# Performance work log

Hardware: AMD Instinct MI355X
Metric: run time of the kernel (lower is better)

The kernel has to match this reference:

```python
import jax, jax.numpy as jnp
import numpy as np

NBINS = (128, 64, 32)
MIN_BIN_WIDTH = 1e-3
MIN_BIN_HEIGHT = 1e-3


def quadratic_spline(inputs, unnorm_widths, unnorm_heights):
    """Piecewise-quadratic CDF spline (nflows-style). inputs: (N,) in [0,1],
    unnorm_widths: (N, nb), unnorm_heights: (N, nb+1). Returns (outputs, logabsdet)."""
    num_bins = unnorm_widths.shape[-1]
    widths = jax.nn.softmax(unnorm_widths, axis=-1)
    widths = MIN_BIN_WIDTH + (1.0 - MIN_BIN_WIDTH * num_bins) * widths
    hexp = jnp.exp(unnorm_heights)
    # normalize piecewise-linear pdf to integrate to 1
    area = jnp.sum(0.5 * (hexp[:, :-1] + hexp[:, 1:]) * widths, axis=-1, keepdims=True)
    heights = hexp / area
    heights = MIN_BIN_HEIGHT + (1.0 - MIN_BIN_HEIGHT) * heights
    bin_cdf = jnp.cumsum(0.5 * (heights[:, :-1] + heights[:, 1:]) * widths, axis=-1)
    bin_left_cdf = jnp.pad(bin_cdf.at[:, -1].set(1.0), ((0, 0), (1, 0)))
    bin_loc = jnp.cumsum(widths, axis=-1)
    bin_locations = jnp.pad(bin_loc.at[:, -1].set(1.0), ((0, 0), (1, 0)))
    bin_idx = jnp.clip(jnp.sum((inputs[:, None] >= bin_locations).astype(jnp.int32), axis=-1) - 1,
                       0, num_bins - 1)[:, None]
    take = lambda t, i: jnp.take_along_axis(t, i, axis=-1)[:, 0]
    loc = take(bin_locations, bin_idx)
    w = take(widths, bin_idx)
    cdf = take(bin_left_cdf, bin_idx)
    hl = take(heights, bin_idx)
    hr = take(heights, bin_idx + 1)
    alpha = (inputs - loc) / w
    outputs = jnp.clip(0.5 * (hr - hl) * w * alpha * alpha + hl * w * alpha + cdf, 0.0, 1.0)
    logabsdet = jnp.log(alpha * (hr - hl) + hl)
    return outputs, logabsdet


def _forward(coordinates, clustering, delta_height_weight, delta_baseline_weight,
             unnormalized_heights, unnormalized_widths, baseline_bias,
             genes_oi, local_gene_ix, local_cellxgene_ix, localcellxgene_ix):
    n_total_genes = delta_baseline_weight.shape[0]
    # decoder
    dhw = delta_height_weight[genes_oi]                            # (G, L, K)
    mixture_delta = jnp.einsum('cl,glk->cgk', clustering, dhw)     # (C, G, K)
    baseline_delta = clustering @ delta_baseline_weight.T          # (C, n_total)
    baseline = jax.nn.softmax(jnp.log(baseline_bias)[None, :] + baseline_delta, axis=-1)
    baseline_cuts = baseline.reshape(-1)[localcellxgene_ix]        # (N,)
    delta = mixture_delta.reshape(-1, mixture_delta.shape[-1])[local_cellxgene_ix]  # (N, K)
    gene_global = genes_oi[local_gene_ix]                          # (N,)
    # quadratic spline stack log_prob (base = Uniform[0,1])
    x = coordinates
    logabsdet = jnp.zeros_like(coordinates)
    ho = 0
    wo = 0
    for n in NBINS:
        uh = unnormalized_heights[:, ho:ho + n][gene_global] + delta[:, ho:ho + n]
        uw = unnormalized_widths[:, wo:wo + n - 1][gene_global]
        x, lad = quadratic_spline(x, uw, uh)
        logabsdet = logabsdet + lad
        ho += n
        wo += n - 1
    likelihood_position = logabsdet
    likelihood_region = jnp.log(baseline_cuts) + jnp.log(jnp.asarray(n_total_genes, jnp.float32))
    elbo = -(likelihood_position + likelihood_region).sum()
    # KL regularization (scales = exp(log 1.0) = 1)
    half_log_2pi = float(0.5 * np.log(2.0 * np.pi))
    mixture_kl = -0.5 * dhw * dhw - half_log_2pi
    baseline_kl = -0.5 * jnp.square(delta_baseline_weight[genes_oi]) - half_log_2pi
    return elbo - mixture_kl.sum() - baseline_kl.sum()


def setup_inputs() -> dict:
    key = jax.random.key(0)
    ks = jax.random.split(key, 10)
    N, C, G, NT, L = 500_000, 1000, 500, 10_000, 16
    K = sum(NBINS)                # 224 heights / delta components
    W = sum(n - 1 for n in NBINS)  # 221 widths
    coordinates = jax.random.uniform(ks[0], (N,), jnp.float32, 1e-4, 1.0 - 1e-4)
    cluster_id = jax.random.randint(ks[1], (C,), 0, L)
    clustering = jax.nn.one_hot(cluster_id, L, dtype=jnp.float32)
    genes_oi = jnp.sort(jax.random.permutation(ks[2], NT)[:G]).astype(jnp.int32)
    cell_ix = jax.random.randint(ks[3], (N,), 0, C)
    local_gene_ix = jax.random.randint(ks[4], (N,), 0, G).astype(jnp.int32)
    local_cellxgene_ix = (cell_ix * G + local_gene_ix).astype(jnp.int32)
    localcellxgene_ix = (cell_ix * NT + genes_oi[local_gene_ix]).astype(jnp.int32)
    delta_height_weight = jax.random.normal(ks[5], (NT, L, K), jnp.float32) * 0.05
    delta_baseline_weight = jax.random.uniform(ks[6], (NT, L), jnp.float32, -0.25, 0.25)
    unnormalized_heights = jax.random.normal(ks[7], (NT, K), jnp.float32) * 0.1
    unnormalized_widths = jax.random.normal(ks[8], (NT, W), jnp.float32) * 0.1
    baseline_bias = jax.random.uniform(ks[9], (NT,), jnp.float32, 1e-5, 1.0)
    return {
        'coordinates': coordinates, 'clustering': clustering,
        'delta_height_weight': delta_height_weight,
        'delta_baseline_weight': delta_baseline_weight,
        'unnormalized_heights': unnormalized_heights,
        'unnormalized_widths': unnormalized_widths,
        'baseline_bias': baseline_bias,
        'genes_oi': genes_oi, 'local_gene_ix': local_gene_ix,
        'local_cellxgene_ix': local_cellxgene_ix,
        'localcellxgene_ix': localcellxgene_ix,
    }


def reference(coordinates, clustering, delta_height_weight, delta_baseline_weight,
              unnormalized_heights, unnormalized_widths, baseline_bias,
              genes_oi, local_gene_ix, local_cellxgene_ix, localcellxgene_ix):
    return _forward(coordinates, clustering, delta_height_weight, delta_baseline_weight,
                    unnormalized_heights, unnormalized_widths, baseline_bias,
                    genes_oi, local_gene_ix, local_cellxgene_ix, localcellxgene_ix)
```

## Files before the change

### kernel.cpp

```cpp
#include <hip/hip_runtime.h>
#include <math.h>


#define CAP 192
static constexpr float  F_MBW = 1e-3f;
static constexpr float  F_MBH = 1e-3f;
static constexpr double D_HL2PI = 0.918938533204672741780329736406;


__global__ void __launch_bounds__(256)
kA(const float* __restrict__ clustering, int* __restrict__ cid,
   double* __restrict__ dpart, int* __restrict__ cnt, int C, int L, int P) {
  int bid = blockIdx.x, tid = threadIdx.x;
  if (bid < 4) {
    int c = bid * 256 + tid;
    if (c < C) {
      const float* row = clustering + (size_t)c * L;
      int best = 0; float bv = row[0];
      for (int l = 1; l < L; ++l) { float v = row[l]; if (v > bv) { bv = v; best = l; } }
      cid[c] = best;
    }
  } else {
    if (bid == 4 && tid < 128) dpart[tid] = 0.0;
    int i = (bid - 4) * 256 + tid;
    if (i < P) cnt[i] = 0;
  }
}

__global__ void __launch_bounds__(256)
kB(const float* __restrict__ coords, const int* __restrict__ lgi,
   const int* __restrict__ lcg, const int* __restrict__ cid,
   const float* __restrict__ bb, const float* __restrict__ dbw,
   int* __restrict__ cnt, float* __restrict__ xs, double* __restrict__ dpart,
   int N, int G, float invG, int L, int NT, int SCAT) {
  int bid = blockIdx.x;
  if (bid < SCAT) {
    int base = bid * 512;
    #pragma unroll
    for (int q = 0; q < 2; ++q) {
      int n = base + q * 256 + threadIdx.x;
      if (n < N) {
        float x = coords[n];
        int cell = (int)(((float)lcg[n] + 0.25f) * invG);
        int pair = lgi[n] * L + cid[cell];
        int pos = atomicAdd(&cnt[pair], 1);
        if (pos < CAP) xs[(size_t)pair * CAP + pos] = x;
      }
    }
  } else {
    int g = (bid - SCAT) * 256 + threadIdx.x;
    float s[16];
    #pragma unroll
    for (int l = 0; l < 16; ++l) s[l] = 0.f;
    if (g < NT) {
      float b = bb[g];
      const float4* row = (const float4*)(dbw + (size_t)g * 16);
      #pragma unroll
      for (int q = 0; q < 4; ++q) {
        float4 v = row[q];
        s[4 * q + 0] = b * expf(v.x); s[4 * q + 1] = b * expf(v.y);
        s[4 * q + 2] = b * expf(v.z); s[4 * q + 3] = b * expf(v.w);
      }
    }
    __shared__ float partl[4][16];
    int lane = threadIdx.x & 63, wv = threadIdx.x >> 6;
    #pragma unroll
    for (int l = 0; l < 16; ++l) {
      float v = s[l];
      for (int off = 32; off; off >>= 1) v += __shfl_xor(v, off);
      if (lane == 0) partl[wv][l] = v;
    }
    __syncthreads();
    if (threadIdx.x < 16) {
      float t = partl[0][threadIdx.x] + partl[1][threadIdx.x]
              + partl[2][threadIdx.x] + partl[3][threadIdx.x];
      atomicAdd(&dpart[threadIdx.x * 8], (double)t);
    }
  }
}

static __device__ __forceinline__ void wscan3(float& x, float& y, float& z, int lane) {
  #pragma unroll
  for (int off = 1; off < 64; off <<= 1) {
    float a = __shfl_up(x, off, 64);
    float b = __shfl_up(y, off, 64);
    float c = __shfl_up(z, off, 64);
    if (lane >= off) { x += a; y += b; z += c; }
  }
}

__global__ void __launch_bounds__(256)
k_pair(const float* __restrict__ uh, const float* __restrict__ uw,
       const float* __restrict__ dhw, const int* __restrict__ genes_oi,
       const float* __restrict__ xs, const int* __restrict__ cnt,
       const float* __restrict__ bb, const float* __restrict__ dbw,
       const double* __restrict__ dpart, float* __restrict__ part,
       int L, int K, int W, int NT) {
  int wv = threadIdx.x >> 6;
  int t  = threadIdx.x & 63;
  int p = blockIdx.x * 4 + wv;
  int g = p / L;
  int cl = p - g * L;
  int gg = genes_oi[g];
  const float* uhg  = uh + (size_t)gg * K;
  const float* uwg  = uw + (size_t)gg * W;
  const float* drow = dhw + ((size_t)gg * L + cl) * K;

  __shared__ float s_loc[4][224];
  __shared__ float s_cdf[4][224];
  __shared__ float s_hh[4][224];
  __shared__ int   grd[4][224];

  const float chh = 1.0f - F_MBH;
  float d2;

  {
    const float cw128 = 1.0f - F_MBW * 127.0f;
    int i0 = 2 * t, i1 = 2 * t + 1;
    float2 dv = *(const float2*)(drow + i0);
    float2 uv = *(const float2*)(uhg + i0);
    d2 = dv.x * dv.x + dv.y * dv.y;
    float h0 = __expf(uv.x + dv.x), h1 = __expf(uv.y + dv.y);
    float h2 = __shfl_down(h0, 1, 64);
    float ew0 = __expf(uwg[i0]);
    float ew1 = (i1 < 127) ? __expf(uwg[i1]) : 0.f;
    float a0 = 0.5f * (h0 + h1);
    float a1 = (i1 < 127) ? 0.5f * (h1 + h2) : 0.f;
    float b0 = a0 * ew0, b1 = a1 * ew1;
    float sew = ew0 + ew1, sa = a0 + a1, sb = b0 + b1;
    wscan3(sew, sa, sb, t);
    float wsum = __shfl(sew, 63);
    float S1   = __shfl(sa, 63);
    float S2   = __shfl(sb, 63);
    float rw = cw128 / wsum;
    float area = F_MBW * S1 + rw * S2;
    float ra = chh / area;
    float E0 = sew - (ew0 + ew1), E1 = E0 + ew0;
    float A0 = sa - (a0 + a1),    A1 = A0 + a0;
    float B0 = sb - (b0 + b1),    B1 = B0 + b0;
    float loc0 = F_MBW * (float)i0 + rw * E0;
    float loc1 = F_MBW * (float)i1 + rw * E1;
    float cdf0 = F_MBH * loc0 + ra * (F_MBW * A0 + rw * B0);
    float cdf1 = F_MBH * loc1 + ra * (F_MBW * A1 + rw * B1);
    if (i1 == 127) { loc1 = 1.0f; cdf1 = 1.0f; }
    s_loc[wv][i0] = loc0; s_cdf[wv][i0] = cdf0; s_hh[wv][i0] = F_MBH + ra * h0;
    s_loc[wv][i1] = loc1; s_cdf[wv][i1] = cdf1; s_hh[wv][i1] = F_MBH + ra * h1;
    float locN = __shfl_down(loc0, 1, 64);
    int j0 = (int)ceilf(loc0 * 128.f);
    int j1 = (int)ceilf(loc1 * 128.f);
    int j2 = (int)ceilf(locN * 128.f);
    j1 = (j1 > 128) ? 128 : j1; j2 = (j2 > 128) ? 128 : j2;
    for (int j = j0; j < j1; ++j) grd[wv][j] = i0;
    if (i1 < 127) for (int j = j1; j < j2; ++j) grd[wv][j] = i1;
  }

  int ho = 128, wo = 127, tb = 128;
  #pragma unroll
  for (int lev = 1; lev < 3; ++lev) {
    const int nbp1 = (lev == 1) ? 64 : 32;
    const int nb = nbp1 - 1;
    const float cwl = 1.0f - F_MBW * (float)nb;
    const float fn = (float)nbp1;
    float dvx = (t < nbp1) ? drow[ho + t] : 0.f;
    d2 += dvx * dvx;
    float hexp = (t < nbp1) ? __expf(uhg[ho + t] + dvx) : 0.f;
    float hn = __shfl_down(hexp, 1, 64);
    float ew = (t < nb) ? __expf(uwg[wo + t]) : 0.f;
    float a  = (t < nb) ? 0.5f * (hexp + hn) : 0.f;
    float b  = a * ew;
    float sew = ew, sa = a, sb = b;
    wscan3(sew, sa, sb, t);
    float wsum = __shfl(sew, nb - 1);
    float S1   = __shfl(sa, nb - 1);
    float S2   = __shfl(sb, nb - 1);
    float rw = cwl / wsum;
    float area = F_MBW * S1 + rw * S2;
    float ra = chh / area;
    float E = sew - ew, A = sa - a, B = sb - b;
    float loc = F_MBW * (float)t + rw * E;
    float cdf = F_MBH * loc + ra * (F_MBW * A + rw * B);
    float h = F_MBH + ra * hexp;
    if (t == nb) { loc = 1.0f; cdf = 1.0f; }
    if (t < nbp1) { s_loc[wv][tb + t] = loc; s_cdf[wv][tb + t] = cdf; s_hh[wv][tb + t] = h; }
    float locN = __shfl_down(loc, 1, 64);
    if (t < nb) {
      int j0 = (int)ceilf(loc * fn);
      int j1 = (int)ceilf(locN * fn);
      j1 = (j1 > nbp1) ? nbp1 : j1;
      for (int j = j0; j < j1; ++j) grd[wv][tb + j] = t;
    }
    ho += nbp1; wo += nb; tb += nbp1;
  }

  const float* sl = s_loc[wv];
  const float* sc = s_cdf[wv];
  const float* sh = s_hh[wv];
  const int*   sg = grd[wv];
  const float* xp = xs + (size_t)p * CAP;
  int m = cnt[p]; if (m > CAP) m = CAP;
  float lad_sum = 0.f;
  for (int i = t; i < m; i += 64) {
    float x = xp[i];
    float lad = 0.f;
    int b2 = 0;
    #pragma unroll
    for (int lev = 0; lev < 3; ++lev) {
      const int nbp1 = (lev == 0) ? 128 : (lev == 1) ? 64 : 32;
      int j = (int)(x * (float)nbp1);
      j = (j > nbp1 - 1) ? (nbp1 - 1) : j;
      int idx = sg[b2 + j];
      while (idx > 0 && sl[b2 + idx] > x) --idx;
      while (idx < nbp1 - 2 && sl[b2 + idx + 1] <= x) ++idx;
      float la = sl[b2 + idx];
      float w  = sl[b2 + idx + 1] - la;
      float cd = sc[b2 + idx];
      float hl = sh[b2 + idx];
      float hr = sh[b2 + idx + 1];
      float alpha = (x - la) / w;
      float dh = hr - hl;
      float outv = (0.5f * dh * alpha + hl) * (w * alpha) + cd;
      x = fminf(fmaxf(outv, 0.f), 1.f);
      lad += __logf(alpha * dh + hl);
      b2 += nbp1;
    }
    lad_sum += lad;
  }
  #pragma unroll
  for (int off = 32; off; off >>= 1) {
    lad_sum += __shfl_xor(lad_sum, off);
    d2      += __shfl_xor(d2, off);
  }
  if (t == 0) {
    float dv = dbw[(size_t)gg * L + cl];
    float rc = __logf(bb[gg]) + dv - __logf((float)dpart[cl * 8]) + __logf((float)NT);
    part[p] = -(lad_sum + (float)m * rc) + 0.5f * (d2 + dv * dv);
  }
}

__global__ void __launch_bounds__(1024)
k_final(const float* __restrict__ part, float* __restrict__ out,
        int P, long long M12) {
  int tid = threadIdx.x;
  double sa = 0.0;
  for (int i = tid; i < P; i += 1024) sa += (double)part[i];
  __shared__ double rA[1024];
  rA[tid] = sa;
  __syncthreads();
  for (int off = 512; off > 0; off >>= 1) {
    if (tid < off) rA[tid] += rA[tid + off];
    __syncthreads();
  }
  if (tid == 0)
    out[0] = (float)(rA[0] + (double)M12 * D_HL2PI);
}

extern "C" void kernel_launch(void* const* d_in, const int* in_sizes, int n_in,
                              void* d_out, int out_size, void* d_ws, size_t ws_size,
                              hipStream_t stream) {
  const float* coords     = (const float*)d_in[0];
  const float* clustering = (const float*)d_in[1];
  const float* dhw        = (const float*)d_in[2];
  const float* dbw        = (const float*)d_in[3];
  const float* uh         = (const float*)d_in[4];
  const float* uw         = (const float*)d_in[5];
  const float* bb         = (const float*)d_in[6];
  const int*   genes_oi   = (const int*)d_in[7];
  const int*   lgi        = (const int*)d_in[8];
  const int*   lcg        = (const int*)d_in[9];

  int N  = in_sizes[0];
  int NT = in_sizes[6];
  int L  = in_sizes[3] / NT;
  int C  = in_sizes[1] / L;
  int K  = in_sizes[4] / NT;
  int W  = in_sizes[5] / NT;
  int G  = in_sizes[7];
  int P  = G * L;
  float invG = 1.0f / (float)G;

  char* ws = (char*)d_ws;
  double* dpart = (double*)ws;
  int*    cid   = (int*)(ws + 4096);
  int*    cnt   = (int*)(ws + 8192);
  float*  part  = (float*)(ws + 40960);
  float*  xs    = (float*)(ws + 131072);

  int SCAT = (N + 511) / 512;
  int LSEB = (NT + 255) / 256;

  hipLaunchKernelGGL(kA, dim3(4 + (P + 255) / 256), dim3(256), 0, stream,
                     clustering, cid, dpart, cnt, C, L, P);
  hipLaunchKernelGGL(kB, dim3(SCAT + LSEB), dim3(256), 0, stream,
                     coords, lgi, lcg, cid, bb, dbw, cnt, xs, dpart,
                     N, G, invG, L, NT, SCAT);
  hipLaunchKernelGGL(k_pair, dim3(P / 4), dim3(256), 0, stream,
                     uh, uw, dhw, genes_oi, xs, cnt, bb, dbw, dpart,
                     part, L, K, W, NT);
  hipLaunchKernelGGL(k_final, dim3(1), dim3(1024), 0, stream,
                     part, (float*)d_out, P,
                     (long long)G * L * K + (long long)G * L);
}
```

Before: 54.85 us.

## Split per-pair scatter counters into four sub-buckets to reduce atomic contention

The scatter now spreads each (gene, cluster) pair's atomic counter across four sub-counters selected by n&3, and each sub-bucket holds up to 64 entries. The aim is to cut contention on hot atomics. The pair kernel then compacts the four sub-buckets into shared memory before evaluating the spline. The trade-offs are more counters to zero, extra shared memory, and a compaction pass. Capacity per sub-bucket is 64, so a skewed distribution could drop points that previously fit under the 192 cap.

```diff
diff --git a/kernel.cpp b/kernel.cpp
--- a/kernel.cpp
+++ b/kernel.cpp
@@ -2,7 +2,7 @@
 #include <math.h>
 
 
-#define CAP 192
+#define CAPS 64
 static constexpr float  F_MBW = 1e-3f;
 static constexpr float  F_MBH = 1e-3f;
 static constexpr double D_HL2PI = 0.918938533204672741780329736406;
@@ -10,7 +10,7 @@
 
 __global__ void __launch_bounds__(256)
 kA(const float* __restrict__ clustering, int* __restrict__ cid,
-   double* __restrict__ dpart, int* __restrict__ cnt, int C, int L, int P) {
+   double* __restrict__ dpart, int* __restrict__ cnt, int C, int L, int P4) {
   int bid = blockIdx.x, tid = threadIdx.x;
   if (bid < 4) {
     int c = bid * 256 + tid;
@@ -23,7 +23,7 @@
   } else {
     if (bid == 4 && tid < 128) dpart[tid] = 0.0;
     int i = (bid - 4) * 256 + tid;
-    if (i < P) cnt[i] = 0;
+    if (i < P4) cnt[i] = 0;
   }
 }
 
@@ -43,8 +43,9 @@
         float x = coords[n];
         int cell = (int)(((float)lcg[n] + 0.25f) * invG);
         int pair = lgi[n] * L + cid[cell];
-        int pos = atomicAdd(&cnt[pair], 1);
-        if (pos < CAP) xs[(size_t)pair * CAP + pos] = x;
+        int s = n & 3;
+        int pos = atomicAdd(&cnt[pair * 4 + s], 1);
+        if (pos < CAPS) xs[(size_t)pair * (4 * CAPS) + s * CAPS + pos] = x;
       }
     }
   } else {
@@ -110,6 +111,7 @@
   __shared__ float s_cdf[4][224];
   __shared__ float s_hh[4][224];
   __shared__ int   grd[4][224];
+  __shared__ float sx[4][4 * CAPS];
 
   const float chh = 1.0f - F_MBH;
   float d2;
@@ -192,15 +194,25 @@
     ho += nbp1; wo += nb; tb += nbp1;
   }
 
+  const float* xp = xs + (size_t)p * (4 * CAPS);
+  int4 c4 = *(const int4*)(cnt + p * 4);
+  int m0 = (c4.x > CAPS) ? CAPS : c4.x;
+  int m1 = (c4.y > CAPS) ? CAPS : c4.y;
+  int m2 = (c4.z > CAPS) ? CAPS : c4.z;
+  int m3 = (c4.w > CAPS) ? CAPS : c4.w;
+  int o1 = m0, o2 = m0 + m1, o3 = o2 + m2, m = o3 + m3;
+  for (int i = t; i < m0; i += 64) sx[wv][i]      = xp[i];
+  for (int i = t; i < m1; i += 64) sx[wv][o1 + i] = xp[CAPS + i];
+  for (int i = t; i < m2; i += 64) sx[wv][o2 + i] = xp[2 * CAPS + i];
+  for (int i = t; i < m3; i += 64) sx[wv][o3 + i] = xp[3 * CAPS + i];
+
   const float* sl = s_loc[wv];
   const float* sc = s_cdf[wv];
   const float* sh = s_hh[wv];
   const int*   sg = grd[wv];
-  const float* xp = xs + (size_t)p * CAP;
-  int m = cnt[p]; if (m > CAP) m = CAP;
   float lad_sum = 0.f;
   for (int i = t; i < m; i += 64) {
-    float x = xp[i];
+    float x = sx[wv][i];
     float lad = 0.f;
     int b2 = 0;
     #pragma unroll
@@ -282,14 +294,15 @@
   double* dpart = (double*)ws;
   int*    cid   = (int*)(ws + 4096);
   int*    cnt   = (int*)(ws + 8192);
-  float*  part  = (float*)(ws + 40960);
-  float*  xs    = (float*)(ws + 131072);
+  float*  part  = (float*)(ws + 139264);
+  float*  xs    = (float*)(ws + 172032);
 
   int SCAT = (N + 511) / 512;
   int LSEB = (NT + 255) / 256;
-
-  hipLaunchKernelGGL(kA, dim3(4 + (P + 255) / 256), dim3(256), 0, stream,
-                     clustering, cid, dpart, cnt, C, L, P);
+  int ZB   = (P * 4 + 255) / 256;
+
+  hipLaunchKernelGGL(kA, dim3(4 + ZB), dim3(256), 0, stream,
+                     clustering, cid, dpart, cnt, C, L, P * 4);
   hipLaunchKernelGGL(kB, dim3(SCAT + LSEB), dim3(256), 0, stream,
                      coords, lgi, lcg, cid, bb, dbw, cnt, xs, dpart,
                      N, G, invG, L, NT, SCAT);
```

New measurement: 61.82 us. 12.7% more time.
